# Kernel tuning notes

Measured on AMD Instinct MI355X. Metric: run time of the kernel, lower is better.

Reference implementation:

```python
import jax, jax.numpy as jnp
import numpy as np

N, E, F, H, L = 10000, 200000, 28, 256, 6
NUM_ATOM, NUM_BOND = 100, 24

def ssp(x):
    # shifted softplus used by SchNet
    return jax.nn.softplus(x) - jnp.log(2.0)

def setup_inputs() -> dict:
    key = jax.random.key(0)
    ks = iter(jax.random.split(key, 64))
    def nrm(shape, scale=0.05):
        return jax.random.normal(next(ks), shape, dtype=jnp.float32) * scale
    inp = {}
    inp['atom_type'] = jax.random.randint(next(ks), (N,), 0, NUM_ATOM)
    inp['r_feat'] = jax.random.normal(next(ks), (N, F), dtype=jnp.float32)
    inp['p_feat'] = jax.random.normal(next(ks), (N, F), dtype=jnp.float32)
    inp['pos'] = jax.random.normal(next(ks), (N, 3), dtype=jnp.float32) * 3.0
    inp['edge_index'] = jax.random.randint(next(ks), (2, E), 0, N)
    inp['edge_type_r'] = jax.random.randint(next(ks), (E,), 0, NUM_BOND)
    inp['edge_type_p'] = jax.random.randint(next(ks), (E,), 0, NUM_BOND)
    # learned parameters
    inp['atom_emb_table'] = nrm((NUM_ATOM, H // 2), 1.0)
    inp['feat_W'] = nrm((F, H // 2))                       # atom_feat_embedding (no bias)
    inp['bond_emb_table'] = nrm((NUM_BOND, H), 1.0)        # edge encoder bond embedding
    inp['edge_mlp_W1'] = nrm((1, H)); inp['edge_mlp_b1'] = jnp.zeros((H,), jnp.float32)
    inp['edge_mlp_W2'] = nrm((H, H)); inp['edge_mlp_b2'] = jnp.zeros((H,), jnp.float32)
    inp['cat_W1'] = nrm((2 * H, H)); inp['cat_b1'] = jnp.zeros((H,), jnp.float32)
    inp['cat_W2'] = nrm((H, H)); inp['cat_b2'] = jnp.zeros((H,), jnp.float32)
    # SchNet interaction blocks, stacked over L layers
    inp['filt_W1'] = nrm((L, H, H)); inp['filt_b1'] = jnp.zeros((L, H), jnp.float32)
    inp['filt_W2'] = nrm((L, H, H)); inp['filt_b2'] = jnp.zeros((L, H), jnp.float32)
    inp['lin1_W'] = nrm((L, H, H))
    inp['lin2_W'] = nrm((L, H, H)); inp['lin2_b'] = jnp.zeros((L, H), jnp.float32)
    inp['lin3_W'] = nrm((L, H, H)); inp['lin3_b'] = jnp.zeros((L, H), jnp.float32)
    # grad_global_dist_mlp: 2H -> H -> H/2 -> 1
    inp['grad_W1'] = nrm((2 * H, H)); inp['grad_b1'] = jnp.zeros((H,), jnp.float32)
    inp['grad_W2'] = nrm((H, H // 2)); inp['grad_b2'] = jnp.zeros((H // 2,), jnp.float32)
    inp['grad_W3'] = nrm((H // 2, 1)); inp['grad_b3'] = jnp.zeros((1,), jnp.float32)
    return inp

def _forward(r_feat, p_feat, pos, atom_emb_table, feat_W, bond_emb_table,
             edge_mlp_W1, edge_mlp_b1, edge_mlp_W2, edge_mlp_b2,
             cat_W1, cat_b1, cat_W2, cat_b2,
             filt_W1, filt_b1, filt_W2, filt_b2,
             lin1_W, lin2_W, lin2_b, lin3_W, lin3_b,
             grad_W1, grad_b1, grad_W2, grad_b2, grad_W3, grad_b3,
             atom_type, edge_index, edge_type_r, edge_type_p):
    src, dst = edge_index[0], edge_index[1]
    # node embedding: z = [atom_emb + feat(r), feat(p) - feat(r)]
    ar = r_feat @ feat_W
    ap = p_feat @ feat_W
    z = jnp.concatenate([atom_emb_table[atom_type] + ar, ap - ar], axis=-1)  # (N, H)
    # edge lengths (E, 1)
    d = pos[src] - pos[dst]
    edge_length = jnp.sqrt(jnp.sum(d * d, axis=-1, keepdims=True) + 1e-12)
    # condensed edge embedding 'bond_w_d': mlp(d) * bond_emb(type), r/p branches, then edge_cat MLP
    d_emb = ssp(edge_length @ edge_mlp_W1 + edge_mlp_b1) @ edge_mlp_W2 + edge_mlp_b2  # (E, H)
    attr_r = d_emb * bond_emb_table[edge_type_r]
    attr_p = d_emb * bond_emb_table[edge_type_p]
    edge_attr = jax.nn.relu(jnp.concatenate([attr_r, attr_p], -1) @ cat_W1 + cat_b1) @ cat_W2 + cat_b2  # (E, H)
    # SchNet encoder: L CFConv interaction blocks with residual
    nn_ = z.shape[0]
    def layer(h, p):
        fW1, fb1, fW2, fb2, l1, l2, l2b, l3, l3b = p
        Wf = ssp(edge_attr @ fW1 + fb1) @ fW2 + fb2            # (E, H) continuous filters
        msg = (h @ l1)[src] * Wf                               # gather + modulate
        agg = jax.ops.segment_sum(msg, dst, num_segments=nn_)  # scatter-add to nodes
        return h + (ssp(agg @ l2 + l2b) @ l3 + l3b), None
    node_attr, _ = jax.lax.scan(layer, z, (filt_W1, filt_b1, filt_W2, filt_b2, lin1_W, lin2_W, lin2_b, lin3_W, lin3_b))
    # assemble_atom_pair_feature: [h_row * h_col, edge_attr] -> (E, 2H)
    h_pair = jnp.concatenate([node_attr[src] * node_attr[dst], edge_attr], axis=-1)
    h = jax.nn.relu(h_pair @ grad_W1 + grad_b1)
    h = jax.nn.relu(h @ grad_W2 + grad_b2)
    edge_inv = h @ grad_W3 + grad_b3                           # (E, 1)
    return edge_inv, edge_length

def reference(atom_type, r_feat, p_feat, pos, edge_index, edge_type_r, edge_type_p,
              atom_emb_table, feat_W, bond_emb_table,
              edge_mlp_W1, edge_mlp_b1, edge_mlp_W2, edge_mlp_b2,
              cat_W1, cat_b1, cat_W2, cat_b2,
              filt_W1, filt_b1, filt_W2, filt_b2,
              lin1_W, lin2_W, lin2_b, lin3_W, lin3_b,
              grad_W1, grad_b1, grad_W2, grad_b2, grad_W3, grad_b3):
    return _forward(r_feat, p_feat, pos, atom_emb_table, feat_W, bond_emb_table,
                    edge_mlp_W1, edge_mlp_b1, edge_mlp_W2, edge_mlp_b2,
                    cat_W1, cat_b1, cat_W2, cat_b2,
                    filt_W1, filt_b1, filt_W2, filt_b2,
                    lin1_W, lin2_W, lin2_b, lin3_W, lin3_b,
                    grad_W1, grad_b1, grad_W2, grad_b2, grad_W3, grad_b3,
                    atom_type, edge_index, edge_type_r, edge_type_p)
```

## Files before the change

### kernel.cpp

```cpp
#include <hip/hip_runtime.h>
#include <hip/hip_bf16.h>
#include <math.h>

#define HDIM 256
#define PSTR 264

typedef unsigned short u16;
typedef short short8 __attribute__((ext_vector_type(8)));
typedef _Float16 f16x8 __attribute__((ext_vector_type(8)));
typedef float f32x4 __attribute__((ext_vector_type(4)));

__device__ __forceinline__ float sspf(float x) {
  const float LOG2E = 1.4426950408889634f, LN2 = 0.6931471805599453f;
  float t = exp2f(-fabsf(x) * LOG2E);
  return fmaxf(x, 0.f) + (log2f(1.f + t) - 1.f) * LN2;
}
__device__ __forceinline__ float bf2f(u16 u) {
  union { unsigned int i; float f; } x; x.i = ((unsigned int)u) << 16; return x.f;
}
__device__ __forceinline__ u16 f2bf(float f) {
  union { float f; unsigned int i; } x; x.f = f;
  unsigned int r = x.i + 0x7FFFu + ((x.i >> 16) & 1u);
  return (u16)(r >> 16);
}
__device__ __forceinline__ u16 f2h_bits(float f) {
  _Float16 h = (_Float16)f;
  return __builtin_bit_cast(unsigned short, h);
}
__device__ __forceinline__ float4 ld4f(const float* p) { return *(const float4*)p; }

__device__ __forceinline__ int iw_idx(int row, int col) {
  return row * 256 + ((((col >> 3) ^ (row & 7)) << 3) | (col & 7));
}
__device__ __forceinline__ int ir_idx(int row, int cchunk) {
  return row * 256 + ((cchunk ^ (row & 7)) << 3);
}

template<int DT>
__device__ __forceinline__ f32x4 mma(short8 a, short8 b, f32x4 c) {
  if constexpr (DT == 0)
    return __builtin_amdgcn_mfma_f32_16x16x32_bf16(a, b, c, 0, 0, 0);
  else
    return __builtin_amdgcn_mfma_f32_16x16x32_f16(__builtin_bit_cast(f16x8, a),
                                                  __builtin_bit_cast(f16x8, b), c, 0, 0, 0);
}

__device__ __forceinline__ void zacc(f32x4 (&acc)[4][4]) {
#pragma unroll
  for (int i = 0; i < 4; ++i)
#pragma unroll
    for (int j = 0; j < 4; ++j) { acc[i][j][0]=0.f; acc[i][j][1]=0.f; acc[i][j][2]=0.f; acc[i][j][3]=0.f; }
}

template<int NSTEPS, int BT_N, int NTW, int DT, bool WRAP8, typename ATR>
__device__ __forceinline__ void gemm44(f32x4 (&acc)[4][4], const u16* __restrict__ bt,
                                       const u16* __restrict__ inter,
                                       int w, int m, int quad, ATR atr) {
#pragma unroll
  for (int ks = 0; ks < NSTEPS; ++ks) {
    short8 bf[NTW];
#pragma unroll
    for (int nt = 0; nt < NTW; ++nt)
      bf[nt] = *(const short8*)(bt + (size_t)ks * (BT_N * 32)
                                + (w * (NTW * 16) + nt * 16 + m) * 32 + quad * 8);
    int kchunk = (WRAP8 ? (ks & 7) : ks) * 4 + quad;
#pragma unroll
    for (int mt = 0; mt < 4; ++mt) {
      short8 af = *(const short8*)&inter[ir_idx(mt * 16 + m, kchunk)];
      af = atr(mt, ks, af);
#pragma unroll
      for (int nt = 0; nt < NTW; ++nt)
        acc[mt][nt] = mma<DT>(af, bf[nt], acc[mt][nt]);
    }
  }
}

template<int NTW, int ACT, int OF>
__device__ __forceinline__ void store_inter44(u16* inter, int w, int m, int quad,
                                              const f32x4 (&acc)[4][4], const float* bias) {
#pragma unroll
  for (int mt = 0; mt < 4; ++mt)
#pragma unroll
    for (int nt = 0; nt < NTW; ++nt) {
      int col = w * (NTW * 16) + nt * 16 + m;
      float bv = bias[col];
#pragma unroll
      for (int r = 0; r < 4; ++r) {
        int row = mt * 16 + quad * 4 + r;
        float x = acc[mt][nt][r] + bv;
        if (ACT == 1) x = fmaxf(x, 0.f);
        else if (ACT == 2) x = sspf(x);
        inter[iw_idx(row, col)] = (OF == 0) ? f2bf(x) : f2h_bits(x);
      }
    }
}

template<int NTW, int ACT>
__device__ __forceinline__ void store_plain44(u16* inter, int w, int m, int quad,
                                              const f32x4 (&acc)[4][4], const float* bias) {
#pragma unroll
  for (int mt = 0; mt < 4; ++mt)
#pragma unroll
    for (int nt = 0; nt < NTW; ++nt) {
      int col = w * (NTW * 16) + nt * 16 + m;
      float bv = bias[col];
#pragma unroll
      for (int r = 0; r < 4; ++r) {
        float x = acc[mt][nt][r] + bv;
        if (ACT == 1) x = fmaxf(x, 0.f);
        inter[(mt * 16 + quad * 4 + r) * PSTR + col] = f2bf(x);
      }
    }
}

__device__ __forceinline__ void copy_out(u16* C, int row0, const u16* inter, int t) {
#pragma unroll
  for (int c = 0; c < 8; ++c) {
    int idx = c * 256 + t;
    int row = idx >> 5, c8 = idx & 31;
    *(short8*)(C + (size_t)(row0 + row) * HDIM + c8 * 8) = *(const short8*)&inter[row * PSTR + c8 * 8];
  }
}

template<int NTW, int ACT, int CM>
__device__ __forceinline__ void store_node44(float* C, int row0, int w, int m, int quad,
                                             const f32x4 (&acc)[4][4], const float* bias, int M) {
#pragma unroll
  for (int mt = 0; mt < 4; ++mt)
#pragma unroll
    for (int nt = 0; nt < NTW; ++nt) {
      int col = w * (NTW * 16) + nt * 16 + m;
      float bv = bias ? bias[col] : 0.f;
#pragma unroll
      for (int r = 0; r < 4; ++r) {
        int row = row0 + mt * 16 + quad * 4 + r;
        if (row < M) {
          float x = acc[mt][nt][r] + bv;
          if (ACT == 2) x = sspf(x);
          size_t idx = (size_t)row * HDIM + col;
          if (CM == 1) x += C[idx];
          C[idx] = x;
        }
      }
    }
}

struct EncArgs {
  const int* se_e; const float* lenp; const float* W1; const float* b1;
  const u16* btA; const float* bA;
  const float* bondT; const int* etr; const int* etp;
  const u16* btB; const float* bB;
  const u16* btC; const float* bC;
  u16* outp;
};
__global__ __launch_bounds__(256, 3) void encoder_k(EncArgs a) {
  __shared__ u16 inter[64 * PSTR];
  __shared__ u16 bondL[24 * 264];
  const int t = threadIdx.x;
  const int w = t >> 6, lane = t & 63, m = lane & 15, quad = lane >> 4;
  const int row0 = blockIdx.x * 64;
  auto idt = [](int, int, short8 v) { return v; };

  for (int i = t; i < 24 * 256; i += 256) {
    int r = i >> 8, c = i & 255;
    bondL[r * 264 + c] = f2h_bits(a.bondT[r * 256 + c]);
  }
  int brv[4], bpv[4];
#pragma unroll
  for (int mt = 0; mt < 4; ++mt) {
    int eo = a.se_e[row0 + mt * 16 + m];
    brv[mt] = a.etr[eo]; bpv[mt] = a.etp[eo];
  }
  {
    int row = t >> 2;
    float len = a.lenp[a.se_e[row0 + row]];
#pragma unroll
    for (int c = 0; c < 8; ++c) {
      int chunk = (t & 3) + c * 4, k = chunk * 8;
      float4 w0 = ld4f(a.W1 + k), w1 = ld4f(a.W1 + k + 4);
      float4 c0 = ld4f(a.b1 + k), c1 = ld4f(a.b1 + k + 4);
      short8 v;
      v[0] = (short)f2bf(sspf(len * w0.x + c0.x)); v[1] = (short)f2bf(sspf(len * w0.y + c0.y));
      v[2] = (short)f2bf(sspf(len * w0.z + c0.z)); v[3] = (short)f2bf(sspf(len * w0.w + c0.w));
      v[4] = (short)f2bf(sspf(len * w1.x + c1.x)); v[5] = (short)f2bf(sspf(len * w1.y + c1.y));
      v[6] = (short)f2bf(sspf(len * w1.z + c1.z)); v[7] = (short)f2bf(sspf(len * w1.w + c1.w));
      *(short8*)&inter[row * 256 + ((chunk ^ (row & 7)) << 3)] = v;
    }
  }
  __syncthreads();
  f32x4 acc[4][4];
  zacc(acc);
  gemm44<8, 256, 4, 0, false>(acc, a.btA, inter, w, m, quad, idt);
  __syncthreads();
  store_inter44<4, 0, 1>(inter, w, m, quad, acc, a.bA);
  __syncthreads();
  zacc(acc);
  auto atrB = [&](int mt, int ks, short8 v) -> short8 {
    int k2 = (ks & 7) * 32 + quad * 8;
    int et = (ks < 8) ? brv[mt] : bpv[mt];
    f16x8 dv = __builtin_bit_cast(f16x8, v);
    f16x8 bd = __builtin_bit_cast(f16x8, *(const short8*)&bondL[et * 264 + k2]);
    return __builtin_bit_cast(short8, dv * bd);
  };
  gemm44<16, 256, 4, 1, true>(acc, a.btB, inter, w, m, quad, atrB);
  __syncthreads();
  store_inter44<4, 1, 0>(inter, w, m, quad, acc, a.bB);
  __syncthreads();
  zacc(acc);
  gemm44<8, 256, 4, 0, false>(acc, a.btC, inter, w, m, quad, idt);
  __syncthreads();
  store_plain44<4, 0>(inter, w, m, quad, acc, a.bC);
  __syncthreads();
  copy_out(a.outp, row0, inter, t);
}

struct FGArgs {
  const u16* eA; const u16* bt1; const float* b1; const u16* bt2; const float* b2;
  const float* hh; const int* se_src; const int* se_dst; float* agg;
};
__global__ __launch_bounds__(256, 3) void fgat_k(FGArgs a) {
  __shared__ u16 inter[64 * PSTR];
  __shared__ int sl[64], dl[64];
  const int t = threadIdx.x;
  const int w = t >> 6, lane = t & 63, m = lane & 15, quad = lane >> 4;
  const int row0 = blockIdx.x * 64;
  auto idt = [](int, int, short8 v) { return v; };
  if (t < 64) { sl[t] = a.se_src[row0 + t]; dl[t] = a.se_dst[row0 + t]; }
  {
    int row = t >> 2;
#pragma unroll
    for (int c = 0; c < 8; ++c) {
      int chunk = (t & 3) + c * 4;
      short8 v = *(const short8*)(a.eA + (size_t)(row0 + row) * HDIM + chunk * 8);
      *(short8*)&inter[row * 256 + ((chunk ^ (row & 7)) << 3)] = v;
    }
  }
  __syncthreads();
  f32x4 acc[4][4];
  zacc(acc);
  gemm44<8, 256, 4, 0, false>(acc, a.bt1, inter, w, m, quad, idt);
  __syncthreads();
  store_inter44<4, 2, 0>(inter, w, m, quad, acc, a.b1);
  __syncthreads();
  zacc(acc);
  gemm44<8, 256, 4, 0, false>(acc, a.bt2, inter, w, m, quad, idt);
  __syncthreads();
  store_plain44<4, 0>(inter, w, m, quad, acc, a.b2);
  __syncthreads();
  float accv = 0.f;
  int cur = dl[0];
  for (int i = 0; i < 64; ++i) {
    int dn = dl[i];
    if (dn != cur) {
      atomicAdd(&a.agg[(size_t)cur * HDIM + t], accv);
      accv = 0.f; cur = dn;
    }
    accv += a.hh[(size_t)sl[i] * HDIM + t] * bf2f(inter[i * PSTR + t]);
  }
  atomicAdd(&a.agg[(size_t)cur * HDIM + t], accv);
}

struct GradArgs {
  const float* h; const int* se_src; const int* se_dst; const int* se_e;
  const u16* eA; const u16* bt1; const float* b1; const u16* bt2; const float* b2;
  const float* W3; const float* b3; float* outp;
};
__global__ __launch_bounds__(256, 3) void gradf_k(GradArgs a) {
  __shared__ u16 inter[64 * 256];
  const int t = threadIdx.x;
  const int w = t >> 6, lane = t & 63, m = lane & 15, quad = lane >> 4;
  const int row0 = blockIdx.x * 64;
  auto idt = [](int, int, short8 v) { return v; };
  {
    int row = t >> 2;
    int s = a.se_src[row0 + row], d = a.se_dst[row0 + row];
#pragma unroll
    for (int c = 0; c < 8; ++c) {
      int chunk = (t & 3) + c * 4, k = chunk * 8;
      const float* xp = a.h + (size_t)s * HDIM + k;
      const float* yp = a.h + (size_t)d * HDIM + k;
      float4 x0 = ld4f(xp), x1 = ld4f(xp + 4);
      float4 y0 = ld4f(yp), y1 = ld4f(yp + 4);
      short8 v;
      v[0] = (short)f2bf(x0.x * y0.x); v[1] = (short)f2bf(x0.y * y0.y);
      v[2] = (short)f2bf(x0.z * y0.z); v[3] = (short)f2bf(x0.w * y0.w);
      v[4] = (short)f2bf(x1.x * y1.x); v[5] = (short)f2bf(x1.y * y1.y);
      v[6] = (short)f2bf(x1.z * y1.z); v[7] = (short)f2bf(x1.w * y1.w);
      *(short8*)&inter[row * 256 + ((chunk ^ (row & 7)) << 3)] = v;
    }
  }
  __syncthreads();
  f32x4 acc[4][4];
  zacc(acc);
  gemm44<8, 256, 4, 0, false>(acc, a.bt1, inter, w, m, quad, idt);
  __syncthreads();
  {
    int row = t >> 2;
#pragma unroll
    for (int c = 0; c < 8; ++c) {
      int chunk = (t & 3) + c * 4;
      short8 v = *(const short8*)(a.eA + (size_t)(row0 + row) * HDIM + chunk * 8);
      *(short8*)&inter[row * 256 + ((chunk ^ (row & 7)) << 3)] = v;
    }
  }
  __syncthreads();
  gemm44<8, 256, 4, 0, false>(acc, a.bt1 + 8 * 256 * 32, inter, w, m, quad, idt);
  __syncthreads();
  store_inter44<4, 1, 0>(inter, w, m, quad, acc, a.b1);
  __syncthreads();
  zacc(acc);
  gemm44<8, 128, 2, 0, false>(acc, a.bt2, inter, w, m, quad, idt);
  float p[4][4];
#pragma unroll
  for (int mt = 0; mt < 4; ++mt) { p[mt][0]=0.f; p[mt][1]=0.f; p[mt][2]=0.f; p[mt][3]=0.f; }
#pragma unroll
  for (int mt = 0; mt < 4; ++mt)
#pragma unroll
    for (int nt = 0; nt < 2; ++nt) {
      int col = w * 32 + nt * 16 + m;
      float w3 = a.W3[col], bv = a.b2[col];
#pragma unroll
      for (int r = 0; r < 4; ++r) p[mt][r] += fmaxf(acc[mt][nt][r] + bv, 0.f) * w3;
    }
  __syncthreads();
  float* red = (float*)inter;
#pragma unroll
  for (int mt = 0; mt < 4; ++mt)
#pragma unroll
    for (int r = 0; r < 4; ++r)
      red[(mt * 16 + quad * 4 + r) * 68 + w * 16 + m] = p[mt][r];
  __syncthreads();
  if (t < 64) {
    float s = a.b3[0];
#pragma unroll
    for (int i = 0; i < 64; ++i) s += red[t * 68 + i];
    a.outp[a.se_e[row0 + t]] = s;
  }
}

struct LinArgs { const float* A; const u16* bt; float* C; int M; };
__global__ __launch_bounds__(256, 3) void lin1_k(LinArgs a) {
  __shared__ u16 inter[64 * 256];
  const int t = threadIdx.x;
  const int w = t >> 6, lane = t & 63, m = lane & 15, quad = lane >> 4;
  const int row0 = blockIdx.x * 64;
  auto idt = [](int, int, short8 v) { return v; };
  {
    int row = t >> 2, grow = row0 + row;
#pragma unroll
    for (int c = 0; c < 8; ++c) {
      int chunk = (t & 3) + c * 4, k = chunk * 8;
      short8 v;
      if (grow < a.M) {
        const float* p = a.A + (size_t)grow * HDIM + k;
        float4 x0 = ld4f(p), x1 = ld4f(p + 4);
        v[0]=(short)f2bf(x0.x); v[1]=(short)f2bf(x0.y); v[2]=(short)f2bf(x0.z); v[3]=(short)f2bf(x0.w);
        v[4]=(short)f2bf(x1.x); v[5]=(short)f2bf(x1.y); v[6]=(short)f2bf(x1.z); v[7]=(short)f2bf(x1.w);
      } else { v = short8{0,0,0,0,0,0,0,0}; }
      *(short8*)&inter[row * 256 + ((chunk ^ (row & 7)) << 3)] = v;
    }
  }
  __syncthreads();
  f32x4 acc[4][4];
  zacc(acc);
  gemm44<8, 256, 4, 0, false>(acc, a.bt, inter, w, m, quad, idt);
  store_node44<4, 0, 0>(a.C, row0, w, m, quad, acc, nullptr, a.M);
}

struct Lin23Args { const float* A; const u16* bt2; const float* b2; const u16* bt3; const float* b3; float* C; int M; };
__global__ __launch_bounds__(256, 3) void lin23_k(Lin23Args a) {
  __shared__ u16 inter[64 * 256];
  const int t = threadIdx.x;
  const int w = t >> 6, lane = t & 63, m = lane & 15, quad = lane >> 4;
  const int row0 = blockIdx.x * 64;
  auto idt = [](int, int, short8 v) { return v; };
  {
    int row = t >> 2, grow = row0 + row;
#pragma unroll
    for (int c = 0; c < 8; ++c) {
      int chunk = (t & 3) + c * 4, k = chunk * 8;
      short8 v;
      if (grow < a.M) {
        const float* p = a.A + (size_t)grow * HDIM + k;
        float4 x0 = ld4f(p), x1 = ld4f(p + 4);
        v[0]=(short)f2bf(x0.x); v[1]=(short)f2bf(x0.y); v[2]=(short)f2bf(x0.z); v[3]=(short)f2bf(x0.w);
        v[4]=(short)f2bf(x1.x); v[5]=(short)f2bf(x1.y); v[6]=(short)f2bf(x1.z); v[7]=(short)f2bf(x1.w);
      } else { v = short8{0,0,0,0,0,0,0,0}; }
      *(short8*)&inter[row * 256 + ((chunk ^ (row & 7)) << 3)] = v;
    }
  }
  __syncthreads();
  f32x4 acc[4][4];
  zacc(acc);
  gemm44<8, 256, 4, 0, false>(acc, a.bt2, inter, w, m, quad, idt);
  __syncthreads();
  store_inter44<4, 2, 0>(inter, w, m, quad, acc, a.b2);
  __syncthreads();
  zacc(acc);
  gemm44<8, 256, 4, 0, false>(acc, a.bt3, inter, w, m, quad, idt);
  store_node44<4, 0, 1>(a.C, row0, w, m, quad, acc, a.b3, a.M);
}

struct WTDesc { const float* src; u16* dst; int K; int Nshift; int fmt; };
struct WTList { WTDesc d[35]; };
__global__ __launch_bounds__(256) void wtrans_k(WTList wl) {
  WTDesc e = wl.d[blockIdx.y];
  int total = e.K << e.Nshift;
  int idx = blockIdx.x * 256 + threadIdx.x;
  if (idx >= total) return;
  int k = idx >> e.Nshift;
  int n = idx & ((1 << e.Nshift) - 1);
  float v = e.src[idx];
  e.dst[((size_t)(k >> 5) << (e.Nshift + 5)) + n * 32 + (k & 31)] = e.fmt ? f2h_bits(v) : f2bf(v);
}

__global__ void node_embed_k(const int* atom_type, const float* r_feat, const float* p_feat,
                             const float* emb, const float* fW, float* z, int N, int F) {
  int n = blockIdx.x;
  int j = threadIdx.x;
  __shared__ float rr[32], pp[32];
  if (j < F) { rr[j] = r_feat[(size_t)n * F + j]; pp[j] = p_feat[(size_t)n * F + j]; }
  __syncthreads();
  float ar = 0.f, ap = 0.f;
  for (int f = 0; f < F; ++f) {
    float wv = fW[f * 128 + j];
    ar += rr[f] * wv;
    ap += pp[f] * wv;
  }
  int at = atom_type[n];
  z[(size_t)n * HDIM + j] = emb[at * 128 + j] + ar;
  z[(size_t)n * HDIM + 128 + j] = ap - ar;
}

__global__ void edge_geom_k(const float* pos, const int* src, const int* dst, float* len_out, int E) {
  int e = blockIdx.x * blockDim.x + threadIdx.x;
  if (e >= E) return;
  int s = src[e], d = dst[e];
  float dx = pos[s * 3 + 0] - pos[d * 3 + 0];
  float dy = pos[s * 3 + 1] - pos[d * 3 + 1];
  float dz = pos[s * 3 + 2] - pos[d * 3 + 2];
  len_out[e] = sqrtf(dx * dx + dy * dy + dz * dz + 1e-12f);
}

__global__ void zero_k(float4* p, int n4) {
  int i = blockIdx.x * 256 + threadIdx.x;
  if (i < n4) p[i] = make_float4(0.f, 0.f, 0.f, 0.f);
}
__global__ void zero_int_k(int* p, int n) {
  int i = blockIdx.x * 256 + threadIdx.x;
  if (i < n) p[i] = 0;
}
__global__ void hist_k(const int* dst, int* cnt, int E) {
  int e = blockIdx.x * 256 + threadIdx.x;
  if (e < E) atomicAdd(&cnt[dst[e]], 1);
}
__global__ __launch_bounds__(256) void scan_k(const int* cnt, int* rowstart, int N) {
  __shared__ int part[256];
  int t = threadIdx.x;
  int chunk = (N + 255) / 256;
  int lo = t * chunk, hi = lo + chunk; if (hi > N) hi = N; if (lo > N) lo = N;
  int s = 0;
  for (int i = lo; i < hi; ++i) s += cnt[i];
  part[t] = s;
  __syncthreads();
  for (int off = 1; off < 256; off <<= 1) {
    int v = (t >= off) ? part[t - off] : 0;
    __syncthreads();
    part[t] += v;
    __syncthreads();
  }
  int run = (t == 0) ? 0 : part[t - 1];
  for (int i = lo; i < hi; ++i) { rowstart[i] = run; run += cnt[i]; }
  if (t == 255) rowstart[N] = run;
}
__global__ void fill_k(const int* src, const int* dst, const int* rowstart, int* cursor,
                       int* se_src, int* se_dst, int* se_e, int E) {
  int e = blockIdx.x * 256 + threadIdx.x;
  if (e >= E) return;
  int d = dst[e];
  int p = atomicAdd(&cursor[d], 1);
  int idx = rowstart[d] + p;
  se_src[idx] = src[e];
  se_dst[idx] = d;
  se_e[idx] = e;
}

extern "C" void kernel_launch(void* const* d_in, const int* in_sizes, int n_in,
                              void* d_out, int out_size, void* d_ws, size_t ws_size,
                              hipStream_t stream) {
  const int* atom_type = (const int*)d_in[0];
  const float* r_feat  = (const float*)d_in[1];
  const float* p_feat  = (const float*)d_in[2];
  const float* pos     = (const float*)d_in[3];
  const int* eidx      = (const int*)d_in[4];
  const int* etype_r   = (const int*)d_in[5];
  const int* etype_p   = (const int*)d_in[6];
  const float* atom_emb = (const float*)d_in[7];
  const float* feat_W   = (const float*)d_in[8];
  const float* bondT    = (const float*)d_in[9];
  const float* e_W1     = (const float*)d_in[10];
  const float* e_b1     = (const float*)d_in[11];
  const float* e_W2     = (const float*)d_in[12];
  const float* e_b2     = (const float*)d_in[13];
  const float* cat_W1   = (const float*)d_in[14];
  const float* cat_b1   = (const float*)d_in[15];
  const float* cat_W2   = (const float*)d_in[16];
  const float* cat_b2   = (const float*)d_in[17];
  const float* filt_W1  = (const float*)d_in[18];
  const float* filt_b1  = (const float*)d_in[19];
  const float* filt_W2  = (const float*)d_in[20];
  const float* filt_b2  = (const float*)d_in[21];
  const float* lin1_W   = (const float*)d_in[22];
  const float* lin2_W   = (const float*)d_in[23];
  const float* lin2_b   = (const float*)d_in[24];
  const float* lin3_W   = (const float*)d_in[25];
  const float* lin3_b   = (const float*)d_in[26];
  const float* grad_W1  = (const float*)d_in[27];
  const float* grad_b1  = (const float*)d_in[28];
  const float* grad_W2  = (const float*)d_in[29];
  const float* grad_b2  = (const float*)d_in[30];
  const float* grad_W3  = (const float*)d_in[31];
  const float* grad_b3  = (const float*)d_in[32];

  const int N = in_sizes[0];
  const int F = in_sizes[1] / N;
  const int E = in_sizes[4] / 2;
  const int L = in_sizes[18] / (HDIM * HDIM);
  const int* srcI = eidx;
  const int* dstI = eidx + E;
  float* out = (float*)d_out;

  const size_t BT_ELEMS = (size_t)(32 * 65536 + 2 * 131072 + 32768);
  size_t need = (size_t)E * HDIM * 2 + 3 * (size_t)N * HDIM * 4 + BT_ELEMS * 2
              + (size_t)(3 * E + 3 * N + 1) * 4 + 64;
  if (ws_size < need) {
    int n4 = (out_size + 3) / 4;
    zero_k<<<(n4 + 255) / 256, 256, 0, stream>>>((float4*)d_out, n4);
    return;
  }
  char* base = (char*)d_ws;
  u16* eA = (u16*)base; base += (size_t)E * HDIM * 2;
  float* h   = (float*)base; base += (size_t)N * HDIM * 4;
  float* hh  = (float*)base; base += (size_t)N * HDIM * 4;
  float* agg = (float*)base; base += (size_t)N * HDIM * 4;
  u16* bt = (u16*)base; base += BT_ELEMS * 2;
  int* se_src = (int*)base; base += (size_t)E * 4;
  int* se_dst = (int*)base; base += (size_t)E * 4;
  int* se_e   = (int*)base; base += (size_t)E * 4;
  int* cnt    = (int*)base; base += (size_t)N * 4;
  int* cursor = (int*)base; base += (size_t)N * 4;
  int* rowstart = (int*)base; base += ((size_t)N + 1) * 4;

  size_t off = 0;
  u16* bt_eW2  = bt + off; off += 65536;
  u16* bt_cat1 = bt + off; off += 131072;
  u16* bt_cat2 = bt + off; off += 65536;
  u16* bt_f1[6]; u16* bt_f2[6]; u16* bt_l1[6]; u16* bt_l2[6]; u16* bt_l3[6];
  for (int l = 0; l < 6; ++l) { bt_f1[l] = bt + off; off += 65536; }
  for (int l = 0; l < 6; ++l) { bt_f2[l] = bt + off; off += 65536; }
  for (int l = 0; l < 6; ++l) { bt_l1[l] = bt + off; off += 65536; }
  for (int l = 0; l < 6; ++l) { bt_l2[l] = bt + off; off += 65536; }
  for (int l = 0; l < 6; ++l) { bt_l3[l] = bt + off; off += 65536; }
  u16* bt_g1 = bt + off; off += 131072;
  u16* bt_g2 = bt + off; off += 32768;

  WTList wl;
  int wi = 0;
  wl.d[wi++] = WTDesc{e_W2, bt_eW2, 256, 8, 0};
  wl.d[wi++] = WTDesc{cat_W1, bt_cat1, 512, 8, 1};
  wl.d[wi++] = WTDesc{cat_W2, bt_cat2, 256, 8, 0};
  for (int l = 0; l < 6; ++l) wl.d[wi++] = WTDesc{filt_W1 + (size_t)l * 65536, bt_f1[l], 256, 8, 0};
  for (int l = 0; l < 6; ++l) wl.d[wi++] = WTDesc{filt_W2 + (size_t)l * 65536, bt_f2[l], 256, 8, 0};
  for (int l = 0; l < 6; ++l) wl.d[wi++] = WTDesc{lin1_W + (size_t)l * 65536, bt_l1[l], 256, 8, 0};
  for (int l = 0; l < 6; ++l) wl.d[wi++] = WTDesc{lin2_W + (size_t)l * 65536, bt_l2[l], 256, 8, 0};
  for (int l = 0; l < 6; ++l) wl.d[wi++] = WTDesc{lin3_W + (size_t)l * 65536, bt_l3[l], 256, 8, 0};
  wl.d[wi++] = WTDesc{grad_W1, bt_g1, 512, 8, 0};
  wl.d[wi++] = WTDesc{grad_W2, bt_g2, 256, 7, 0};
  wtrans_k<<<dim3(512, 35), 256, 0, stream>>>(wl);

  const int EB = E / 64;
  const int NBK = (N + 63) / 64;
  const int EBLK = (E + 255) / 256;
  const int NZ4 = N * HDIM / 4;

  zero_int_k<<<(2 * N + 255) / 256, 256, 0, stream>>>(cnt, 2 * N);
  hist_k<<<EBLK, 256, 0, stream>>>(dstI, cnt, E);
  scan_k<<<1, 256, 0, stream>>>(cnt, rowstart, N);
  fill_k<<<EBLK, 256, 0, stream>>>(srcI, dstI, rowstart, cursor, se_src, se_dst, se_e, E);

  node_embed_k<<<N, 128, 0, stream>>>(atom_type, r_feat, p_feat, atom_emb, feat_W, h, N, F);
  edge_geom_k<<<EBLK, 256, 0, stream>>>(pos, srcI, dstI, out + E, E);

  EncArgs ea;
  ea.se_e = se_e; ea.lenp = out + E; ea.W1 = e_W1; ea.b1 = e_b1;
  ea.btA = bt_eW2; ea.bA = e_b2;
  ea.bondT = bondT; ea.etr = etype_r; ea.etp = etype_p;
  ea.btB = bt_cat1; ea.bB = cat_b1;
  ea.btC = bt_cat2; ea.bC = cat_b2;
  ea.outp = eA;
  encoder_k<<<EB, 256, 0, stream>>>(ea);

  for (int l = 0; l < L; ++l) {
    const size_t bo = (size_t)l * HDIM;
    LinArgs la{h, bt_l1[l], hh, N};
    lin1_k<<<NBK, 256, 0, stream>>>(la);
    zero_k<<<(NZ4 + 255) / 256, 256, 0, stream>>>((float4*)agg, NZ4);
    FGArgs fg{eA, bt_f1[l], filt_b1 + bo, bt_f2[l], filt_b2 + bo, hh, se_src, se_dst, agg};
    fgat_k<<<EB, 256, 0, stream>>>(fg);
    Lin23Args l23{agg, bt_l2[l], lin2_b + bo, bt_l3[l], lin3_b + bo, h, N};
    lin23_k<<<NBK, 256, 0, stream>>>(l23);
  }

  GradArgs ga;
  ga.h = h; ga.se_src = se_src; ga.se_dst = se_dst; ga.se_e = se_e;
  ga.eA = eA; ga.bt1 = bt_g1; ga.b1 = grad_b1; ga.bt2 = bt_g2; ga.b2 = grad_b2;
  ga.W3 = grad_W3; ga.b3 = grad_b3; ga.outp = out;
  gradf_k<<<EB, 256, 0, stream>>>(ga);
}
```

Measured before the change: 1.921 ms.

## Stage weight k-slices through shared memory and drop fp16 encoder path

Each GEMM step now loads a 32-wide k-slice of the transposed weights cooperatively into a padded LDS buffer, with barriers, instead of each wave loading its B fragments straight from global memory. The encoder's fp16 bond-embedding multiply and f16 MFMA are replaced by bf16, reading bond rows from global memory, and the padded output staging is replaced by the swizzled layout. This is meant to cut redundant global/L2 weight traffic across waves. It adds two barriers per k-step and more LDS per block, which may reduce occupancy, and changes the precision of the encoder path.

```diff
diff --git a/kernel.cpp b/kernel.cpp
--- a/kernel.cpp
+++ b/kernel.cpp
@@ -3,11 +3,9 @@
 #include <math.h>
 
 #define HDIM 256
-#define PSTR 264
 
 typedef unsigned short u16;
 typedef short short8 __attribute__((ext_vector_type(8)));
-typedef _Float16 f16x8 __attribute__((ext_vector_type(8)));
 typedef float f32x4 __attribute__((ext_vector_type(4)));
 
 __device__ __forceinline__ float sspf(float x) {
@@ -23,10 +21,6 @@
   unsigned int r = x.i + 0x7FFFu + ((x.i >> 16) & 1u);
   return (u16)(r >> 16);
 }
-__device__ __forceinline__ u16 f2h_bits(float f) {
-  _Float16 h = (_Float16)f;
-  return __builtin_bit_cast(unsigned short, h);
-}
 __device__ __forceinline__ float4 ld4f(const float* p) { return *(const float4*)p; }
 
 __device__ __forceinline__ int iw_idx(int row, int col) {
@@ -36,15 +30,6 @@
   return row * 256 + ((cchunk ^ (row & 7)) << 3);
 }
 
-template<int DT>
-__device__ __forceinline__ f32x4 mma(short8 a, short8 b, f32x4 c) {
-  if constexpr (DT == 0)
-    return __builtin_amdgcn_mfma_f32_16x16x32_bf16(a, b, c, 0, 0, 0);
-  else
-    return __builtin_amdgcn_mfma_f32_16x16x32_f16(__builtin_bit_cast(f16x8, a),
-                                                  __builtin_bit_cast(f16x8, b), c, 0, 0, 0);
-}
-
 __device__ __forceinline__ void zacc(f32x4 (&acc)[4][4]) {
 #pragma unroll
   for (int i = 0; i < 4; ++i)
@@ -52,30 +37,42 @@
     for (int j = 0; j < 4; ++j) { acc[i][j][0]=0.f; acc[i][j][1]=0.f; acc[i][j][2]=0.f; acc[i][j][3]=0.f; }
 }
 
-template<int NSTEPS, int BT_N, int NTW, int DT, bool WRAP8, typename ATR>
-__device__ __forceinline__ void gemm44(f32x4 (&acc)[4][4], const u16* __restrict__ bt,
-                                       const u16* __restrict__ inter,
-                                       int w, int m, int quad, ATR atr) {
+template<int NSTEPS, int BT_N, int NTW, bool WRAP8, typename ATR>
+__device__ __forceinline__ void gemm44s(f32x4 (&acc)[4][4], const u16* __restrict__ bt,
+                                        u16* __restrict__ Bs, const u16* __restrict__ inter,
+                                        int t, int w, int m, int quad, ATR atr) {
 #pragma unroll
   for (int ks = 0; ks < NSTEPS; ++ks) {
-    short8 bf[NTW];
-#pragma unroll
-    for (int nt = 0; nt < NTW; ++nt)
-      bf[nt] = *(const short8*)(bt + (size_t)ks * (BT_N * 32)
-                                + (w * (NTW * 16) + nt * 16 + m) * 32 + quad * 8);
+    __syncthreads();
+    if (BT_N == 256 || t < BT_N) {
+      const u16* g = bt + (size_t)ks * (BT_N * 32) + t * 32;
+      short8 c0 = *(const short8*)(g);
+      short8 c1 = *(const short8*)(g + 8);
+      short8 c2 = *(const short8*)(g + 16);
+      short8 c3 = *(const short8*)(g + 24);
+      u16* dp = Bs + t * 40;
+      *(short8*)(dp) = c0; *(short8*)(dp + 8) = c1;
+      *(short8*)(dp + 16) = c2; *(short8*)(dp + 24) = c3;
+    }
+    __syncthreads();
     int kchunk = (WRAP8 ? (ks & 7) : ks) * 4 + quad;
+    short8 af[4];
 #pragma unroll
     for (int mt = 0; mt < 4; ++mt) {
-      short8 af = *(const short8*)&inter[ir_idx(mt * 16 + m, kchunk)];
-      af = atr(mt, ks, af);
-#pragma unroll
-      for (int nt = 0; nt < NTW; ++nt)
-        acc[mt][nt] = mma<DT>(af, bf[nt], acc[mt][nt]);
-    }
-  }
-}
-
-template<int NTW, int ACT, int OF>
+      af[mt] = *(const short8*)&inter[ir_idx(mt * 16 + m, kchunk)];
+      af[mt] = atr(mt, ks, af[mt]);
+    }
+#pragma unroll
+    for (int nt = 0; nt < NTW; ++nt) {
+      short8 bf = *(const short8*)&Bs[(w * (NTW * 16) + nt * 16 + m) * 40 + quad * 8];
+#pragma unroll
+      for (int mt = 0; mt < 4; ++mt)
+        acc[mt][nt] = __builtin_amdgcn_mfma_f32_16x16x32_bf16(af[mt], bf, acc[mt][nt], 0, 0, 0);
+    }
+  }
+}
+
+template<int NTW, int ACT>
 __device__ __forceinline__ void store_inter44(u16* inter, int w, int m, int quad,
                                               const f32x4 (&acc)[4][4], const float* bias) {
 #pragma unroll
@@ -90,25 +87,7 @@
         float x = acc[mt][nt][r] + bv;
         if (ACT == 1) x = fmaxf(x, 0.f);
         else if (ACT == 2) x = sspf(x);
-        inter[iw_idx(row, col)] = (OF == 0) ? f2bf(x) : f2h_bits(x);
-      }
-    }
-}
-
-template<int NTW, int ACT>
-__device__ __forceinline__ void store_plain44(u16* inter, int w, int m, int quad,
-                                              const f32x4 (&acc)[4][4], const float* bias) {
-#pragma unroll
-  for (int mt = 0; mt < 4; ++mt)
-#pragma unroll
-    for (int nt = 0; nt < NTW; ++nt) {
-      int col = w * (NTW * 16) + nt * 16 + m;
-      float bv = bias[col];
-#pragma unroll
-      for (int r = 0; r < 4; ++r) {
-        float x = acc[mt][nt][r] + bv;
-        if (ACT == 1) x = fmaxf(x, 0.f);
-        inter[(mt * 16 + quad * 4 + r) * PSTR + col] = f2bf(x);
+        inter[iw_idx(row, col)] = f2bf(x);
       }
     }
 }
@@ -118,7 +97,8 @@
   for (int c = 0; c < 8; ++c) {
     int idx = c * 256 + t;
     int row = idx >> 5, c8 = idx & 31;
-    *(short8*)(C + (size_t)(row0 + row) * HDIM + c8 * 8) = *(const short8*)&inter[row * PSTR + c8 * 8];
+    int src = (c8 ^ (row & 7)) << 3;
+    *(short8*)(C + (size_t)(row0 + row) * HDIM + c8 * 8) = *(const short8*)&inter[row * 256 + src];
   }
 }
 
@@ -154,17 +134,12 @@
   u16* outp;
 };
 __global__ __launch_bounds__(256, 3) void encoder_k(EncArgs a) {
-  __shared__ u16 inter[64 * PSTR];
-  __shared__ u16 bondL[24 * 264];
+  __shared__ u16 Bs[256 * 40];
+  __shared__ u16 inter[64 * 256];
   const int t = threadIdx.x;
   const int w = t >> 6, lane = t & 63, m = lane & 15, quad = lane >> 4;
   const int row0 = blockIdx.x * 64;
   auto idt = [](int, int, short8 v) { return v; };
-
-  for (int i = t; i < 24 * 256; i += 256) {
-    int r = i >> 8, c = i & 255;
-    bondL[r * 264 + c] = f2h_bits(a.bondT[r * 256 + c]);
-  }
   int brv[4], bpv[4];
 #pragma unroll
   for (int mt = 0; mt < 4; ++mt) {
@@ -187,29 +162,31 @@
       *(short8*)&inter[row * 256 + ((chunk ^ (row & 7)) << 3)] = v;
     }
   }
-  __syncthreads();
   f32x4 acc[4][4];
   zacc(acc);
-  gemm44<8, 256, 4, 0, false>(acc, a.btA, inter, w, m, quad, idt);
-  __syncthreads();
-  store_inter44<4, 0, 1>(inter, w, m, quad, acc, a.bA);
-  __syncthreads();
+  gemm44s<8, 256, 4, false>(acc, a.btA, Bs, inter, t, w, m, quad, idt);
+  __syncthreads();
+  store_inter44<4, 0>(inter, w, m, quad, acc, a.bA);
   zacc(acc);
   auto atrB = [&](int mt, int ks, short8 v) -> short8 {
     int k2 = (ks & 7) * 32 + quad * 8;
     int et = (ks < 8) ? brv[mt] : bpv[mt];
-    f16x8 dv = __builtin_bit_cast(f16x8, v);
-    f16x8 bd = __builtin_bit_cast(f16x8, *(const short8*)&bondL[et * 264 + k2]);
-    return __builtin_bit_cast(short8, dv * bd);
+    const float* brow = a.bondT + (size_t)et * 256 + k2;
+    float4 q0 = ld4f(brow), q1 = ld4f(brow + 4);
+    short8 o;
+    o[0] = (short)f2bf(bf2f((u16)v[0]) * q0.x); o[1] = (short)f2bf(bf2f((u16)v[1]) * q0.y);
+    o[2] = (short)f2bf(bf2f((u16)v[2]) * q0.z); o[3] = (short)f2bf(bf2f((u16)v[3]) * q0.w);
+    o[4] = (short)f2bf(bf2f((u16)v[4]) * q1.x); o[5] = (short)f2bf(bf2f((u16)v[5]) * q1.y);
+    o[6] = (short)f2bf(bf2f((u16)v[6]) * q1.z); o[7] = (short)f2bf(bf2f((u16)v[7]) * q1.w);
+    return o;
   };
-  gemm44<16, 256, 4, 1, true>(acc, a.btB, inter, w, m, quad, atrB);
-  __syncthreads();
-  store_inter44<4, 1, 0>(inter, w, m, quad, acc, a.bB);
-  __syncthreads();
-  zacc(acc);
-  gemm44<8, 256, 4, 0, false>(acc, a.btC, inter, w, m, quad, idt);
-  __syncthreads();
-  store_plain44<4, 0>(inter, w, m, quad, acc, a.bC);
+  gemm44s<16, 256, 4, true>(acc, a.btB, Bs, inter, t, w, m, quad, atrB);
+  __syncthreads();
+  store_inter44<4, 1>(inter, w, m, quad, acc, a.bB);
+  zacc(acc);
+  gemm44s<8, 256, 4, false>(acc, a.btC, Bs, inter, t, w, m, quad, idt);
+  __syncthreads();
+  store_inter44<4, 0>(inter, w, m, quad, acc, a.bC);
   __syncthreads();
   copy_out(a.outp, row0, inter, t);
 }
@@ -219,7 +196,8 @@
   const float* hh; const int* se_src; const int* se_dst; float* agg;
 };
 __global__ __launch_bounds__(256, 3) void fgat_k(FGArgs a) {
-  __shared__ u16 inter[64 * PSTR];
+  __shared__ u16 Bs[256 * 40];
+  __shared__ u16 inter[64 * 256];
   __shared__ int sl[64], dl[64];
   const int t = threadIdx.x;
   const int w = t >> 6, lane = t & 63, m = lane & 15, quad = lane >> 4;
@@ -235,17 +213,15 @@
       *(short8*)&inter[row * 256 + ((chunk ^ (row & 7)) << 3)] = v;
     }
   }
-  __syncthreads();
   f32x4 acc[4][4];
   zacc(acc);
-  gemm44<8, 256, 4, 0, false>(acc, a.bt1, inter, w, m, quad, idt);
-  __syncthreads();
-  store_inter44<4, 2, 0>(inter, w, m, quad, acc, a.b1);
-  __syncthreads();
-  zacc(acc);
-  gemm44<8, 256, 4, 0, false>(acc, a.bt2, inter, w, m, quad, idt);
-  __syncthreads();
-  store_plain44<4, 0>(inter, w, m, quad, acc, a.b2);
+  gemm44s<8, 256, 4, false>(acc, a.bt1, Bs, inter, t, w, m, quad, idt);
+  __syncthreads();
+  store_inter44<4, 2>(inter, w, m, quad, acc, a.b1);
+  zacc(acc);
+  gemm44s<8, 256, 4, false>(acc, a.bt2, Bs, inter, t, w, m, quad, idt);
+  __syncthreads();
+  store_inter44<4, 0>(inter, w, m, quad, acc, a.b2);
   __syncthreads();
   float accv = 0.f;
   int cur = dl[0];
@@ -255,7 +231,8 @@
       atomicAdd(&a.agg[(size_t)cur * HDIM + t], accv);
       accv = 0.f; cur = dn;
     }
-    accv += a.hh[(size_t)sl[i] * HDIM + t] * bf2f(inter[i * PSTR + t]);
+    int src = ((((t >> 3) ^ (i & 7)) << 3) | (t & 7));
+    accv += a.hh[(size_t)sl[i] * HDIM + t] * bf2f(inter[i * 256 + src]);
   }
   atomicAdd(&a.agg[(size_t)cur * HDIM + t], accv);
 }
@@ -266,6 +243,7 @@
   const float* W3; const float* b3; float* outp;
 };
 __global__ __launch_bounds__(256, 3) void gradf_k(GradArgs a) {
+  __shared__ u16 Bs[256 * 40];
   __shared__ u16 inter[64 * 256];
   const int t = threadIdx.x;
   const int w = t >> 6, lane = t & 63, m = lane & 15, quad = lane >> 4;
@@ -289,10 +267,9 @@
       *(short8*)&inter[row * 256 + ((chunk ^ (row & 7)) << 3)] = v;
     }
   }
-  __syncthreads();
   f32x4 acc[4][4];
   zacc(acc);
-  gemm44<8, 256, 4, 0, false>(acc, a.bt1, inter, w, m, quad, idt);
+  gemm44s<8, 256, 4, false>(acc, a.bt1, Bs, inter, t, w, m, quad, idt);
   __syncthreads();
   {
     int row = t >> 2;
@@ -303,13 +280,11 @@
       *(short8*)&inter[row * 256 + ((chunk ^ (row & 7)) << 3)] = v;
     }
   }
-  __syncthreads();
-  gemm44<8, 256, 4, 0, false>(acc, a.bt1 + 8 * 256 * 32, inter, w, m, quad, idt);
-  __syncthreads();
-  store_inter44<4, 1, 0>(inter, w, m, quad, acc, a.b1);
-  __syncthreads();
-  zacc(acc);
-  gemm44<8, 128, 2, 0, false>(acc, a.bt2, inter, w, m, quad, idt);
+  gemm44s<8, 256, 4, false>(acc, a.bt1 + 8 * 256 * 32, Bs, inter, t, w, m, quad, idt);
+  __syncthreads();
+  store_inter44<4, 1>(inter, w, m, quad, acc, a.b1);
+  zacc(acc);
+  gemm44s<8, 128, 2, false>(acc, a.bt2, Bs, inter, t, w, m, quad, idt);
   float p[4][4];
 #pragma unroll
   for (int mt = 0; mt < 4; ++mt) { p[mt][0]=0.f; p[mt][1]=0.f; p[mt][2]=0.f; p[mt][3]=0.f; }
@@ -340,6 +315,7 @@
 
 struct LinArgs { const float* A; const u16* bt; float* C; int M; };
 __global__ __launch_bounds__(256, 3) void lin1_k(LinArgs a) {
+  __shared__ u16 Bs[256 * 40];
   __shared__ u16 inter[64 * 256];
   const int t = threadIdx.x;
   const int w = t >> 6, lane = t & 63, m = lane & 15, quad = lane >> 4;
@@ -360,15 +336,15 @@
       *(short8*)&inter[row * 256 + ((chunk ^ (row & 7)) << 3)] = v;
     }
   }
-  __syncthreads();
   f32x4 acc[4][4];
   zacc(acc);
-  gemm44<8, 256, 4, 0, false>(acc, a.bt, inter, w, m, quad, idt);
+  gemm44s<8, 256, 4, false>(acc, a.bt, Bs, inter, t, w, m, quad, idt);
   store_node44<4, 0, 0>(a.C, row0, w, m, quad, acc, nullptr, a.M);
 }
 
 struct Lin23Args { const float* A; const u16* bt2; const float* b2; const u16* bt3; const float* b3; float* C; int M; };
 __global__ __launch_bounds__(256, 3) void lin23_k(Lin23Args a) {
+  __shared__ u16 Bs[256 * 40];
   __shared__ u16 inter[64 * 256];
   const int t = threadIdx.x;
   const int w = t >> 6, lane = t & 63, m = lane & 15, quad = lane >> 4;
@@ -389,19 +365,17 @@
       *(short8*)&inter[row * 256 + ((chunk ^ (row & 7)) << 3)] = v;
     }
   }
-  __syncthreads();
   f32x4 acc[4][4];
   zacc(acc);
-  gemm44<8, 256, 4, 0, false>(acc, a.bt2, inter, w, m, quad, idt);
-  __syncthreads();
-  store_inter44<4, 2, 0>(inter, w, m, quad, acc, a.b2);
-  __syncthreads();
-  zacc(acc);
-  gemm44<8, 256, 4, 0, false>(acc, a.bt3, inter, w, m, quad, idt);
+  gemm44s<8, 256, 4, false>(acc, a.bt2, Bs, inter, t, w, m, quad, idt);
+  __syncthreads();
+  store_inter44<4, 2>(inter, w, m, quad, acc, a.b2);
+  zacc(acc);
+  gemm44s<8, 256, 4, false>(acc, a.bt3, Bs, inter, t, w, m, quad, idt);
   store_node44<4, 0, 1>(a.C, row0, w, m, quad, acc, a.b3, a.M);
 }
 
-struct WTDesc { const float* src; u16* dst; int K; int Nshift; int fmt; };
+struct WTDesc { const float* src; u16* dst; int K; int Nshift; };
 struct WTList { WTDesc d[35]; };
 __global__ __launch_bounds__(256) void wtrans_k(WTList wl) {
   WTDesc e = wl.d[blockIdx.y];
@@ -410,8 +384,7 @@
   if (idx >= total) return;
   int k = idx >> e.Nshift;
   int n = idx & ((1 << e.Nshift) - 1);
-  float v = e.src[idx];
-  e.dst[((size_t)(k >> 5) << (e.Nshift + 5)) + n * 32 + (k & 31)] = e.fmt ? f2h_bits(v) : f2bf(v);
+  e.dst[((size_t)(k >> 5) << (e.Nshift + 5)) + n * 32 + (k & 31)] = f2bf(e.src[idx]);
 }
 
 __global__ void node_embed_k(const int* atom_type, const float* r_feat, const float* p_feat,
@@ -566,16 +539,16 @@
 
   WTList wl;
   int wi = 0;
-  wl.d[wi++] = WTDesc{e_W2, bt_eW2, 256, 8, 0};
-  wl.d[wi++] = WTDesc{cat_W1, bt_cat1, 512, 8, 1};
-  wl.d[wi++] = WTDesc{cat_W2, bt_cat2, 256, 8, 0};
-  for (int l = 0; l < 6; ++l) wl.d[wi++] = WTDesc{filt_W1 + (size_t)l * 65536, bt_f1[l], 256, 8, 0};
-  for (int l = 0; l < 6; ++l) wl.d[wi++] = WTDesc{filt_W2 + (size_t)l * 65536, bt_f2[l], 256, 8, 0};
-  for (int l = 0; l < 6; ++l) wl.d[wi++] = WTDesc{lin1_W + (size_t)l * 65536, bt_l1[l], 256, 8, 0};
-  for (int l = 0; l < 6; ++l) wl.d[wi++] = WTDesc{lin2_W + (size_t)l * 65536, bt_l2[l], 256, 8, 0};
-  for (int l = 0; l < 6; ++l) wl.d[wi++] = WTDesc{lin3_W + (size_t)l * 65536, bt_l3[l], 256, 8, 0};
-  wl.d[wi++] = WTDesc{grad_W1, bt_g1, 512, 8, 0};
-  wl.d[wi++] = WTDesc{grad_W2, bt_g2, 256, 7, 0};
+  wl.d[wi++] = WTDesc{e_W2, bt_eW2, 256, 8};
+  wl.d[wi++] = WTDesc{cat_W1, bt_cat1, 512, 8};
+  wl.d[wi++] = WTDesc{cat_W2, bt_cat2, 256, 8};
+  for (int l = 0; l < 6; ++l) wl.d[wi++] = WTDesc{filt_W1 + (size_t)l * 65536, bt_f1[l], 256, 8};
+  for (int l = 0; l < 6; ++l) wl.d[wi++] = WTDesc{filt_W2 + (size_t)l * 65536, bt_f2[l], 256, 8};
+  for (int l = 0; l < 6; ++l) wl.d[wi++] = WTDesc{lin1_W + (size_t)l * 65536, bt_l1[l], 256, 8};
+  for (int l = 0; l < 6; ++l) wl.d[wi++] = WTDesc{lin2_W + (size_t)l * 65536, bt_l2[l], 256, 8};
+  for (int l = 0; l < 6; ++l) wl.d[wi++] = WTDesc{lin3_W + (size_t)l * 65536, bt_l3[l], 256, 8};
+  wl.d[wi++] = WTDesc{grad_W1, bt_g1, 512, 8};
+  wl.d[wi++] = WTDesc{grad_W2, bt_g2, 256, 7};
   wtrans_k<<<dim3(512, 35), 256, 0, stream>>>(wl);
 
   const int EB = E / 64;
```

Measured after the change: 2.283 ms. 18.8% more time.
